# Performance work log

Hardware: AMD Instinct MI355X
Metric: run time of the kernel (lower is better)

Reference implementation:

```python
import jax, jax.numpy as jnp
import numpy as np

D_MODEL = 1024
N_HEAD = 16
D_K = D_MODEL // N_HEAD


def setup_inputs() -> dict:
    key = jax.random.key(0)
    ks = jax.random.split(key, 11)
    B, S = 2, 2048
    scale = 1.0 / np.sqrt(D_MODEL)
    inp = {
        "q": jax.random.normal(ks[0], (B, S, D_MODEL), jnp.float32),
        "k": jax.random.normal(ks[1], (B, S, D_MODEL), jnp.float32),
        "v": jax.random.normal(ks[2], (B, S, D_MODEL), jnp.float32),
        "Wq": jax.random.normal(ks[3], (D_MODEL, D_MODEL), jnp.float32) * scale,
        "bq": jnp.zeros((D_MODEL,), jnp.float32),
        "Wk": jax.random.normal(ks[4], (D_MODEL, D_MODEL), jnp.float32) * scale,
        "bk": jnp.zeros((D_MODEL,), jnp.float32),
        "Wv": jax.random.normal(ks[5], (D_MODEL, D_MODEL), jnp.float32) * scale,
        "bv": jnp.zeros((D_MODEL,), jnp.float32),
        "Wo": jax.random.normal(ks[6], (D_MODEL, D_MODEL), jnp.float32) * scale,
        "bo": jnp.zeros((D_MODEL,), jnp.float32),
    }
    return inp


def _split_heads(x):
    B, S, _ = x.shape
    return x.reshape(B, S, N_HEAD, D_K).transpose(0, 2, 1, 3)  # [B,H,S,Dk]


def reference(q, k, v, Wq, bq, Wk, bk, Wv, bv, Wo, bo):
    # Linear projections (torch Linear: x @ W.T + b)
    qh = _split_heads(q @ Wq.T + bq)
    kh = _split_heads(k @ Wk.T + bk)
    vh = _split_heads(v @ Wv.T + bv)
    # naive scaled dot-product attention, full [B,H,S,S] scores
    score = jnp.einsum("bhqd,bhkd->bhqk", qh, kh) / jnp.sqrt(jnp.float32(D_K))
    attn = jax.nn.softmax(score, axis=-1)
    out = jnp.einsum("bhqk,bhkd->bhqd", attn, vh)
    B, H, S, Dk = out.shape
    out = out.transpose(0, 2, 1, 3).reshape(B, S, H * Dk)
    return out @ Wo.T + bo
```

## Files before the change

kernel.cpp:

```cpp
#include <hip/hip_runtime.h>

typedef __attribute__((ext_vector_type(8))) short bh8;
typedef __attribute__((ext_vector_type(4))) float fx4;
typedef __attribute__((ext_vector_type(16))) float fx16;
typedef __attribute__((ext_vector_type(4))) unsigned short us4;
typedef unsigned short u16;

__device__ __forceinline__ u16 f2bf(float x) {
  unsigned u = __float_as_uint(x);
  u += 0x7fffu + ((u >> 16) & 1u);
  return (u16)(u >> 16);
}

__device__ __forceinline__ void async16(const void* g, void* l) {
  __builtin_amdgcn_global_load_lds(
      (const __attribute__((address_space(1))) void*)g,
      (__attribute__((address_space(3))) void*)l,
      16, 0, 0);
}

__global__ __launch_bounds__(256) void k_convert(
    const float* __restrict__ q, const float* __restrict__ k, const float* __restrict__ v,
    const float* __restrict__ wq, const float* __restrict__ wk,
    const float* __restrict__ wv, const float* __restrict__ wo,
    u16* __restrict__ dst) {
  size_t gid = (size_t)blockIdx.x * 256 + threadIdx.x;
  size_t e4 = gid * 4;
  const float* src; size_t off;
  if (e4 < 4194304)        { src = q;  off = e4; }
  else if (e4 < 8388608)   { src = k;  off = e4 - 4194304; }
  else if (e4 < 12582912)  { src = v;  off = e4 - 8388608; }
  else if (e4 < 13631488)  { src = wq; off = e4 - 12582912; }
  else if (e4 < 14680064)  { src = wk; off = e4 - 13631488; }
  else if (e4 < 15728640)  { src = wv; off = e4 - 14680064; }
  else                     { src = wo; off = e4 - 15728640; }
  float4 f = *(const float4*)(src + off);
  us4 o; o.x = f2bf(f.x); o.y = f2bf(f.y); o.z = f2bf(f.z); o.w = f2bf(f.w);
  *(us4*)(dst + e4) = o;
}

__device__ __forceinline__ void gemm_stage(const u16* __restrict__ A, const u16* __restrict__ B,
                                           char* lds, int bufbase, int m0, int n0, int kt, int tid) {
  int wb16 = (tid & 0xC0) * 16;
  #pragma unroll
  for (int i = 0; i < 2; ++i) {
    int cl = i * 256 + tid;
    int row = cl >> 2, ch = cl & 3;
    int sch = ch ^ (row & 3);
    const char* ga = (const char*)(A + (size_t)(m0 + row) * 1024 + kt * 32) + sch * 16;
    async16(ga, lds + bufbase + i * 4096 + wb16);
    const char* gb = (const char*)(B + (size_t)(n0 + row) * 1024 + kt * 32) + sch * 16;
    async16(gb, lds + bufbase + 8192 + i * 4096 + wb16);
  }
}

__device__ __forceinline__ void gemm_core(const u16* __restrict__ A, const u16* __restrict__ Bw,
                                          const float* __restrict__ bias, void* Cout, int mode,
                                          float scl, char* lds) {
  int tid = threadIdx.x;
  int lane = tid & 63, w = tid >> 6, g = lane >> 4, cc = lane & 15;
  int wr = w >> 1, wc = w & 1;
  int m0 = blockIdx.y * 128, n0 = blockIdx.x * 128;
  fx4 acc[4][4] = {};
  gemm_stage(A, Bw, lds, 0, m0, n0, 0, tid);
  for (int kt = 0; kt < 32; ++kt) {
    __syncthreads();
    if (kt + 1 < 32) gemm_stage(A, Bw, lds, ((kt + 1) & 1) * 16384, m0, n0, kt + 1, tid);
    const char* bA = lds + (kt & 1) * 16384;
    const char* bB = bA + 8192;
    bh8 af[4], bf[4];
    #pragma unroll
    for (int mf = 0; mf < 4; ++mf) {
      int row = wr * 64 + mf * 16 + cc;
      af[mf] = *(const bh8*)(bA + row * 64 + ((g ^ (row & 3)) * 16));
    }
    #pragma unroll
    for (int nf = 0; nf < 4; ++nf) {
      int row = wc * 64 + nf * 16 + cc;
      bf[nf] = *(const bh8*)(bB + row * 64 + ((g ^ (row & 3)) * 16));
    }
    #pragma unroll
    for (int mf = 0; mf < 4; ++mf)
      #pragma unroll
      for (int nf = 0; nf < 4; ++nf)
        acc[mf][nf] = __builtin_amdgcn_mfma_f32_16x16x32_bf16(af[mf], bf[nf], acc[mf][nf], 0, 0, 0);
  }
  #pragma unroll
  for (int mf = 0; mf < 4; ++mf) {
    #pragma unroll
    for (int nf = 0; nf < 4; ++nf) {
      fx4 a = acc[mf][nf];
      int row = m0 + wr * 64 + mf * 16 + g * 4;
      int col = n0 + wc * 64 + nf * 16 + cc;
      float bv = bias[col];
      if (mode == 0) {
        u16* C = (u16*)Cout;
        #pragma unroll
        for (int r = 0; r < 4; ++r) C[(size_t)(row + r) * 1024 + col] = f2bf((a[r] + bv) * scl);
      } else if (mode == 1) {
        float* C = (float*)Cout;
        #pragma unroll
        for (int r = 0; r < 4; ++r) C[(size_t)(row + r) * 1024 + col] = (a[r] + bv) * scl;
      } else {
        u16* C = (u16*)Cout;
        us4 o;
        #pragma unroll
        for (int r = 0; r < 4; ++r) o[r] = f2bf((a[r] + bv) * scl);
        int bb = row >> 11;
        *(us4*)(C + (size_t)(bb * 1024 + col) * 2048 + (row & 2047)) = o;
      }
    }
  }
}

__global__ __launch_bounds__(256) void k_gemm_qkv(
    const u16* __restrict__ qb, const u16* __restrict__ kb, const u16* __restrict__ vb,
    const u16* __restrict__ wqb, const u16* __restrict__ wkb, const u16* __restrict__ wvb,
    const float* __restrict__ bq, const float* __restrict__ bk, const float* __restrict__ bv,
    u16* __restrict__ Qp, u16* __restrict__ Kp, u16* __restrict__ Vt) {
  __shared__ __align__(16) char lds[32768];
  int z = blockIdx.z;
  const u16* A = (z == 0) ? qb : (z == 1) ? kb : vb;
  const u16* B = (z == 0) ? wqb : (z == 1) ? wkb : wvb;
  const float* bias = (z == 0) ? bq : (z == 1) ? bk : bv;
  void* C = (z == 0) ? (void*)Qp : (z == 1) ? (void*)Kp : (void*)Vt;
  float scl = (z == 0) ? 0.18033688f : 1.0f;
  gemm_core(A, B, bias, C, (z == 2) ? 2 : 0, scl, lds);
}

__global__ __launch_bounds__(256) void k_gemm_out(
    const u16* __restrict__ Ob, const u16* __restrict__ wob,
    const float* __restrict__ bo, float* __restrict__ out) {
  __shared__ __align__(16) char lds[32768];
  gemm_core(Ob, wob, bo, out, 1, 1.0f, lds);
}

__global__ __launch_bounds__(256) void k_attn(
    const u16* __restrict__ Qp, const u16* __restrict__ Kp,
    const u16* __restrict__ Vt, u16* __restrict__ O) {
  __shared__ __align__(16) char lds[65536];
  int tid = threadIdx.x;
  int lane = tid & 63, w = tid >> 6, ql = lane & 31, hi = lane >> 5;
  int lin = blockIdx.y * 16 + blockIdx.x;
  int xcd = lin & 7, slot = lin >> 3;
  int bh = xcd * 4 + (slot >> 4), qtile = slot & 15;
  int b = bh >> 4, h = bh & 15;
  int q0 = qtile * 128 + w * 32;
  size_t qrow = (size_t)b * 2048 + q0 + ql;
  bh8 qf[4];
  #pragma unroll
  for (int ds = 0; ds < 4; ++ds)
    qf[ds] = *(const bh8*)(Qp + qrow * 1024 + h * 64 + ds * 16 + hi * 8);

  int r0 = tid >> 3;
  int gr0 = (r0 & 19) | (((r0 >> 2) & 1) << 3) | (((r0 >> 3) & 1) << 2);
  int sK = (tid & 7) ^ (r0 & 7);
  const char* gK = (const char*)(Kp + (size_t)(b * 2048 + gr0) * 1024 + h * 64) + sK * 16;
  int vr0 = tid >> 4;
  int sV = (tid & 15) ^ (vr0 & 7);
  const char* gV = (const char*)(Vt + ((size_t)(b * 1024 + h * 64 + vr0)) * 2048) + sV * 16;
  int wb16 = (tid & 0xC0) * 16;

  int x7 = ql & 7;
  int kbase = ql * 128, vbase = ql * 256;
  int kc[4], vc[8];
  #pragma unroll
  for (int ds = 0; ds < 4; ++ds) kc[ds] = ((ds * 2 + hi) ^ x7) * 16;
  #pragma unroll
  for (int ks = 0; ks < 8; ++ks) vc[ks] = ((ks * 2 + hi) ^ x7) * 16;

  float lpart = 0.f;
  fx16 ot[2] = {};
  #pragma unroll
  for (int i = 0; i < 4; ++i) {
    async16(gK + i * 65536, lds + i * 4096 + wb16);
    async16(gV + i * 65536, lds + 16384 + i * 4096 + wb16);
  }
  gK += 262144; gV += 256;

  for (int t = 0; t < 16; ++t) {
    __syncthreads();
    if (t + 1 < 16) {
      int bb = ((t + 1) & 1) << 15;
      #pragma unroll
      for (int i = 0; i < 4; ++i) {
        async16(gK + i * 65536, lds + bb + i * 4096 + wb16);
        async16(gV + i * 65536, lds + bb + 16384 + i * 4096 + wb16);
      }
      gK += 262144; gV += 256;
    }
    const char* bK = lds + ((t & 1) << 15);
    const char* bV = bK + 16384;
    fx16 st[4] = {};
    #pragma unroll
    for (int kk = 0; kk < 4; ++kk)
      #pragma unroll
      for (int ds = 0; ds < 4; ++ds)
        st[kk] = __builtin_amdgcn_mfma_f32_32x32x16_bf16(
            *(const bh8*)(bK + kk * 4096 + kbase + kc[ds]), qf[ds], st[kk], 0, 0, 0);
    bh8 Pf[8];
    #pragma unroll
    for (int kk = 0; kk < 4; ++kk) {
      #pragma unroll
      for (int m = 0; m < 2; ++m) {
        float p[8];
        #pragma unroll
        for (int e = 0; e < 8; ++e) p[e] = __builtin_amdgcn_exp2f(st[kk][8 * m + e]);
        lpart += ((p[0] + p[1]) + (p[2] + p[3])) + ((p[4] + p[5]) + (p[6] + p[7]));
        unsigned u0, u1, u2, u3;
        asm("v_cvt_pk_bf16_f32 %0, %1, %2" : "=v"(u0) : "v"(p[0]), "v"(p[1]));
        asm("v_cvt_pk_bf16_f32 %0, %1, %2" : "=v"(u1) : "v"(p[2]), "v"(p[3]));
        asm("v_cvt_pk_bf16_f32 %0, %1, %2" : "=v"(u2) : "v"(p[4]), "v"(p[5]));
        asm("v_cvt_pk_bf16_f32 %0, %1, %2" : "=v"(u3) : "v"(p[6]), "v"(p[7]));
        union { unsigned u[4]; bh8 v; } pu;
        pu.u[0] = u0; pu.u[1] = u1; pu.u[2] = u2; pu.u[3] = u3;
        Pf[kk * 2 + m] = pu.v;
      }
    }
    #pragma unroll
    for (int dt = 0; dt < 2; ++dt)
      #pragma unroll
      for (int ks = 0; ks < 8; ++ks)
        ot[dt] = __builtin_amdgcn_mfma_f32_32x32x16_bf16(
            *(const bh8*)(bV + dt * 8192 + vbase + vc[ks]), Pf[ks], ot[dt], 0, 0, 0);
  }
  float lsum = lpart + __shfl_xor(lpart, 32);
  float inv = 1.f / lsum;
  #pragma unroll
  for (int dt = 0; dt < 2; ++dt)
    #pragma unroll
    for (int j = 0; j < 4; ++j) {
      us4 o4;
      #pragma unroll
      for (int i = 0; i < 4; ++i) o4[i] = f2bf(ot[dt][4 * j + i] * inv);
      *(us4*)(O + qrow * 1024 + h * 64 + dt * 32 + j * 8 + hi * 4) = o4;
    }
}

extern "C" void kernel_launch(void* const* d_in, const int* in_sizes, int n_in,
                              void* d_out, int out_size, void* d_ws, size_t ws_size,
                              hipStream_t stream) {
  const float* q  = (const float*)d_in[0];
  const float* k  = (const float*)d_in[1];
  const float* v  = (const float*)d_in[2];
  const float* Wq = (const float*)d_in[3];
  const float* bq = (const float*)d_in[4];
  const float* Wk = (const float*)d_in[5];
  const float* bk = (const float*)d_in[6];
  const float* Wv = (const float*)d_in[7];
  const float* bv = (const float*)d_in[8];
  const float* Wo = (const float*)d_in[9];
  const float* bo = (const float*)d_in[10];
  u16* ws  = (u16*)d_ws;
  u16* qb  = ws;
  u16* kb  = qb + 4194304;
  u16* vb  = kb + 4194304;
  u16* wqb = vb + 4194304;
  u16* wkb = wqb + 1048576;
  u16* wvb = wkb + 1048576;
  u16* wob = wvb + 1048576;
  u16* Qp  = wob + 1048576;
  u16* Kp  = Qp + 4194304;
  u16* Vt  = Kp + 4194304;
  u16* Ob  = qb;

  k_convert<<<dim3(16384), 256, 0, stream>>>(q, k, v, Wq, Wk, Wv, Wo, qb);
  k_gemm_qkv<<<dim3(8, 32, 3), 256, 0, stream>>>(qb, kb, vb, wqb, wkb, wvb, bq, bk, bv, Qp, Kp, Vt);
  k_attn<<<dim3(16, 32), 256, 0, stream>>>(Qp, Kp, Vt, Ob);
  k_gemm_out<<<dim3(8, 32, 1), 256, 0, stream>>>(Ob, wob, bo, (float*)d_out);
}
```

Before: 125.9 us.

## Software-pipeline PV matmul one tile behind QK to overlap exp with MFMA

Restructures the attention loop so that the P·V MFMAs for tile t-1 run after the QK^T and exp of tile t. The previous V tile is preloaded into registers before the next async load overwrites its buffer. It also adds s_setprio around the MFMA blocks so waves interleave matrix and exponent work. The cost is higher register pressure from holding V fragments and two P sets, plus an extra epilogue iteration.

```diff
diff --git a/kernel.cpp b/kernel.cpp
--- a/kernel.cpp
+++ b/kernel.cpp
@@ -171,6 +171,8 @@
 
   float lpart = 0.f;
   fx16 ot[2] = {};
+  bh8 pf[8];
+
   #pragma unroll
   for (int i = 0; i < 4; ++i) {
     async16(gK + i * 65536, lds + i * 4096 + wb16);
@@ -180,25 +182,36 @@
 
   for (int t = 0; t < 16; ++t) {
     __syncthreads();
+    const char* bufc = lds + ((t & 1) << 15);
+    char* bufp = lds + (((t + 1) & 1) << 15);
+    bh8 va[2][8];
+    if (t) {
+      #pragma unroll
+      for (int dt = 0; dt < 2; ++dt)
+        #pragma unroll
+        for (int ks = 0; ks < 8; ++ks)
+          va[dt][ks] = *(const bh8*)(bufp + 16384 + dt * 8192 + vbase + vc[ks]);
+      asm volatile("s_waitcnt lgkmcnt(0)" ::: "memory");
+      __builtin_amdgcn_sched_barrier(0);
+    }
     if (t + 1 < 16) {
-      int bb = ((t + 1) & 1) << 15;
       #pragma unroll
       for (int i = 0; i < 4; ++i) {
-        async16(gK + i * 65536, lds + bb + i * 4096 + wb16);
-        async16(gV + i * 65536, lds + bb + 16384 + i * 4096 + wb16);
+        async16(gK + i * 65536, bufp + i * 4096 + wb16);
+        async16(gV + i * 65536, bufp + 16384 + i * 4096 + wb16);
       }
       gK += 262144; gV += 256;
     }
-    const char* bK = lds + ((t & 1) << 15);
-    const char* bV = bK + 16384;
     fx16 st[4] = {};
+    __builtin_amdgcn_s_setprio(1);
     #pragma unroll
     for (int kk = 0; kk < 4; ++kk)
       #pragma unroll
       for (int ds = 0; ds < 4; ++ds)
         st[kk] = __builtin_amdgcn_mfma_f32_32x32x16_bf16(
-            *(const bh8*)(bK + kk * 4096 + kbase + kc[ds]), qf[ds], st[kk], 0, 0, 0);
-    bh8 Pf[8];
+            *(const bh8*)(bufc + kk * 4096 + kbase + kc[ds]), qf[ds], st[kk], 0, 0, 0);
+    __builtin_amdgcn_s_setprio(0);
+    bh8 pfn[8];
     #pragma unroll
     for (int kk = 0; kk < 4; ++kk) {
       #pragma unroll
@@ -214,15 +227,34 @@
         asm("v_cvt_pk_bf16_f32 %0, %1, %2" : "=v"(u3) : "v"(p[6]), "v"(p[7]));
         union { unsigned u[4]; bh8 v; } pu;
         pu.u[0] = u0; pu.u[1] = u1; pu.u[2] = u2; pu.u[3] = u3;
-        Pf[kk * 2 + m] = pu.v;
+        pfn[kk * 2 + m] = pu.v;
       }
     }
+    if (t) {
+      __builtin_amdgcn_s_setprio(1);
+      #pragma unroll
+      for (int dt = 0; dt < 2; ++dt)
+        #pragma unroll
+        for (int ks = 0; ks < 8; ++ks)
+          ot[dt] = __builtin_amdgcn_mfma_f32_32x32x16_bf16(va[dt][ks], pf[ks], ot[dt], 0, 0, 0);
+      __builtin_amdgcn_s_setprio(0);
+    }
+    #pragma unroll
+    for (int ks = 0; ks < 8; ++ks) pf[ks] = pfn[ks];
+  }
+  {
+    const char* bV = lds + (1 << 15) + 16384;
+    bh8 va[2][8];
     #pragma unroll
     for (int dt = 0; dt < 2; ++dt)
       #pragma unroll
       for (int ks = 0; ks < 8; ++ks)
-        ot[dt] = __builtin_amdgcn_mfma_f32_32x32x16_bf16(
-            *(const bh8*)(bV + dt * 8192 + vbase + vc[ks]), Pf[ks], ot[dt], 0, 0, 0);
+        va[dt][ks] = *(const bh8*)(bV + dt * 8192 + vbase + vc[ks]);
+    #pragma unroll
+    for (int dt = 0; dt < 2; ++dt)
+      #pragma unroll
+      for (int ks = 0; ks < 8; ++ks)
+        ot[dt] = __builtin_amdgcn_mfma_f32_32x32x16_bf16(va[dt][ks], pf[ks], ot[dt], 0, 0, 0);
   }
   float lsum = lpart + __shfl_xor(lpart, 32);
   float inv = 1.f / lsum;
```

After: 140.1 us. 11.2% more time.
